# Kernel optimization log

Measured on AMD Instinct MI355X. Metric: run time of the kernel, lower is better.

## Reference

```python
import jax, jax.numpy as jnp
import numpy as np

EPS = 1e-8

def unit_projection(x):
    # project each embedding vector so its Fourier coefficients have unit magnitude
    f = jnp.fft.fft(x, axis=-1)
    f = f / jnp.maximum(jnp.abs(f), EPS)
    return jnp.real(jnp.fft.ifft(f, axis=-1))

def bind(a, b):
    return jnp.fft.irfft(jnp.fft.rfft(a, axis=-1) * jnp.fft.rfft(b, axis=-1), n=a.shape[-1], axis=-1)

def unbind(s, k):
    # k is unit-magnitude in Fourier domain, so its inverse is its conjugate
    return jnp.fft.irfft(jnp.fft.rfft(s, axis=-1) * jnp.conj(jnp.fft.rfft(k, axis=-1)), n=s.shape[-1], axis=-1)

def layer_norm(x, g, b):
    mu = jnp.mean(x, axis=-1, keepdims=True)
    var = jnp.var(x, axis=-1, keepdims=True)
    return (x - mu) * jax.lax.rsqrt(var + 1e-5) * g + b

def setup_inputs():
    key = jax.random.key(0)
    ks = jax.random.split(key, 12)
    B, S, D = 4, 2048, 1024
    sc = 1.0 / np.sqrt(D)
    inp = {
        'x': jax.random.normal(ks[0], (B, S, D), jnp.float32),
        'Wq': jax.random.normal(ks[1], (D, D), jnp.float32) * sc,
        'bq': jnp.zeros((D,), jnp.float32),
        'Wk': jax.random.normal(ks[2], (D, D), jnp.float32) * sc,
        'bk': jnp.zeros((D,), jnp.float32),
        'Wv': jax.random.normal(ks[3], (D, D), jnp.float32) * sc,
        'bv': jnp.zeros((D,), jnp.float32),
        'ln1_g': jnp.ones((D,), jnp.float32), 'ln1_b': jnp.zeros((D,), jnp.float32),
        'ln2_g': jnp.ones((D,), jnp.float32), 'ln2_b': jnp.zeros((D,), jnp.float32),
        'W1': jax.random.normal(ks[4], (D, 4 * D), jnp.float32) * sc,
        'b1': jnp.zeros((4 * D,), jnp.float32),
        'W2': jax.random.normal(ks[5], (4 * D, D), jnp.float32) * (1.0 / np.sqrt(4 * D)),
        'b2': jnp.zeros((D,), jnp.float32),
    }
    return inp

def reference(x, Wq, bq, Wk, bk, Wv, bv, ln1_g, ln1_b, ln2_g, ln2_b, W1, b1, W2, b2):
    h = layer_norm(x, ln1_g, ln1_b)
    q = unit_projection(h @ Wq + bq)
    k = unit_projection(h @ Wk + bk)
    v = unit_projection(h @ Wv + bv)
    s = jnp.cumsum(bind(k, v), axis=1)  # causal prefix-sum over sequence
    mixed = unbind(s, q)
    x = x + mixed  # dropout=0.0
    h2 = layer_norm(x, ln2_g, ln2_b)
    mlp = jax.nn.gelu(h2 @ W1 + b1, approximate=False) @ W2 + b2
    return x + mlp
```

## Files before the change

kernel.cpp:

```cpp
#include <hip/hip_runtime.h>
#include <cstdint>
#include <cstddef>

#define DD 1024
#define SSEQ 2048
#define NB 4
#define MROWS 8192
#define FBINS 513
#define FPAD 520
#define WFP 1152
#define NQKV 3456
#define NHID 4096
#define NCHUNK 64
#define SCHUNK 32

typedef _Float16 f16_t;
typedef _Float16 f16x8 __attribute__((ext_vector_type(8)));
typedef float f32x4 __attribute__((ext_vector_type(4)));

__device__ __forceinline__ float2 cmul(float2 a, float2 b) {
  return make_float2(a.x * b.x - a.y * b.y, a.x * b.y + a.y * b.x);
}

__device__ __forceinline__ void async_cp16(const void* g, void* l) {
  __builtin_amdgcn_global_load_lds(
      (const __attribute__((address_space(1))) void*)g,
      (__attribute__((address_space(3))) void*)l, 16, 0, 0);
}

__device__ __forceinline__ void fft1024(float2* bufA, float2* bufB,
                                        const float2* tw, int tid) {
  float2* s = bufA;
  float2* d = bufB;
  for (int m = 1; m < 1024; m <<= 1) {
#pragma unroll
    for (int r2 = 0; r2 < 2; ++r2) {
      int u = tid + r2 * 256;
      int k = u & (m - 1);
      int jm = u - k;
      float2 c0 = s[u];
      float2 c1 = s[u + 512];
      float2 wt = tw[jm];
      float2 su = make_float2(c0.x + c1.x, c0.y + c1.y);
      float2 df = make_float2(c0.x - c1.x, c0.y - c1.y);
      float2 pr = cmul(wt, df);
      d[2 * jm + k] = su;
      d[2 * jm + k + m] = pr;
    }
    __syncthreads();
    float2* tmp = s; s = d; d = tmp;
  }
}

__global__ __launch_bounds__(256) void wfft_k(
    const float* __restrict__ Wq, const float* __restrict__ Wk,
    const float* __restrict__ Wv, float* __restrict__ WfAll) {
  __shared__ float2 tw[512];
  __shared__ float2 bufA[1024];
  __shared__ float2 bufB[1024];
  const int tid = threadIdx.x;
  const int p = blockIdx.x >> 10, k = blockIdx.x & 1023;
  const float* W = (p == 0) ? Wq : ((p == 1) ? Wk : Wv);
  for (int t = tid; t < 512; t += 256) {
    float ang = -6.2831853071795864769f * (float)t * (1.0f / 1024.0f);
    tw[t] = make_float2(cosf(ang), sinf(ang));
  }
  const float* src = W + (size_t)k * DD;
  for (int t = tid; t < 1024; t += 256) bufA[t] = make_float2(src[t], 0.f);
  __syncthreads();
  fft1024(bufA, bufB, tw, tid);
  float* dst = WfAll + ((size_t)p * DD + k) * WFP;
  for (int t = tid; t <= 512; t += 256) {
    float2 f = bufA[t];
    dst[2 * t] = f.x;
    dst[2 * t + 1] = f.y;
  }
  for (int j = 1026 + tid; j < WFP; j += 256) dst[j] = 0.f;
}

__global__ __launch_bounds__(256) void bfft_k(
    const float* __restrict__ bq, const float* __restrict__ bk,
    const float* __restrict__ bv, float* __restrict__ biasC) {
  __shared__ float2 tw[512];
  __shared__ float2 bufA[1024];
  __shared__ float2 bufB[1024];
  const int tid = threadIdx.x;
  const int p = blockIdx.x;
  const float* bsrc = (p == 0) ? bq : ((p == 1) ? bk : bv);
  for (int t = tid; t < 512; t += 256) {
    float ang = -6.2831853071795864769f * (float)t * (1.0f / 1024.0f);
    tw[t] = make_float2(cosf(ang), sinf(ang));
  }
  for (int t = tid; t < 1024; t += 256) bufA[t] = make_float2(bsrc[t], 0.f);
  __syncthreads();
  fft1024(bufA, bufB, tw, tid);
  float* dst = biasC + (size_t)p * WFP;
  for (int t = tid; t <= 512; t += 256) {
    float2 f = bufA[t];
    dst[2 * t] = f.x;
    dst[2 * t + 1] = f.y;
  }
  for (int j = 1026 + tid; j < WFP; j += 256) dst[j] = 0.f;
}

__global__ __launch_bounds__(256) void transpose_cast_k(
    const float* __restrict__ W, f16_t* __restrict__ Wt, int K, int N) {
  __shared__ float tile[32][33];
  const int tx = threadIdx.x & 31, ty = threadIdx.x >> 5;
  const int n0 = blockIdx.x * 32, k0 = blockIdx.y * 32;
#pragma unroll
  for (int i = 0; i < 32; i += 8)
    tile[ty + i][tx] = W[(size_t)(k0 + ty + i) * N + n0 + tx];
  __syncthreads();
#pragma unroll
  for (int i = 0; i < 32; i += 8)
    Wt[(size_t)(n0 + ty + i) * K + k0 + tx] = (f16_t)tile[tx][ty + i];
}

__global__ __launch_bounds__(256) void transpose_cast2_k(
    const float* __restrict__ W, f16_t* __restrict__ WtH,
    f16_t* __restrict__ WtL, int K, int N) {
  __shared__ float tile[32][33];
  const int tx = threadIdx.x & 31, ty = threadIdx.x >> 5;
  const int n0 = blockIdx.x * 32, k0 = blockIdx.y * 32;
#pragma unroll
  for (int i = 0; i < 32; i += 8)
    tile[ty + i][tx] = W[(size_t)(k0 + ty + i) * N + n0 + tx];
  __syncthreads();
#pragma unroll
  for (int i = 0; i < 32; i += 8) {
    float val = tile[tx][ty + i];
    f16_t hi = (f16_t)val;
    f16_t lo = (f16_t)(val - (float)hi);
    size_t idx = (size_t)(n0 + ty + i) * K + k0 + tx;
    WtH[idx] = hi;
    WtL[idx] = lo;
  }
}

__global__ __launch_bounds__(256) void ln_cast2_k(
    const float* __restrict__ x, const float* __restrict__ g,
    const float* __restrict__ b, f16_t* __restrict__ hH,
    f16_t* __restrict__ hL) {
  const int row = blockIdx.x, tid = threadIdx.x;
  __shared__ float red[8];
  const float* xr = x + (size_t)row * DD;
  float v[4], ls = 0.f, lq = 0.f;
#pragma unroll
  for (int i = 0; i < 4; ++i) {
    v[i] = xr[i * 256 + tid];
    ls += v[i];
    lq += v[i] * v[i];
  }
#pragma unroll
  for (int o = 32; o > 0; o >>= 1) {
    ls += __shfl_down(ls, o);
    lq += __shfl_down(lq, o);
  }
  const int lane = tid & 63, w = tid >> 6;
  if (lane == 0) { red[w] = ls; red[w + 4] = lq; }
  __syncthreads();
  const float S = red[0] + red[1] + red[2] + red[3];
  const float Q = red[4] + red[5] + red[6] + red[7];
  const float mean = S * (1.f / 1024.f);
  const float var = Q * (1.f / 1024.f) - mean * mean;
  const float rs = rsqrtf(var + 1e-5f);
#pragma unroll
  for (int i = 0; i < 4; ++i) {
    int n = i * 256 + tid;
    float val = (v[i] - mean) * rs * g[n] + b[n];
    f16_t hi = (f16_t)val;
    hH[(size_t)row * DD + n] = hi;
    hL[(size_t)row * DD + n] = (f16_t)(val - (float)hi);
  }
}

__global__ __launch_bounds__(256, 2) void gemm_qkv_k(
    const f16_t* __restrict__ Ahi, const f16_t* __restrict__ Alo,
    const f16_t* __restrict__ Bhi, const float* __restrict__ bias,
    float* __restrict__ outF) {
  __shared__ alignas(16) f16_t AsH[128 * 64];
  __shared__ alignas(16) f16_t AsL[128 * 64];
  __shared__ alignas(16) f16_t BsH[128 * 64];
  const int tid = threadIdx.x;
  const int lane = tid & 63;
  const int w = tid >> 6;
  const int wm = w >> 1, wn = w & 1;

  const int lin = blockIdx.x;
  const int s = (lin & 7) * 216 + (lin >> 3);
  const int g = s / 108;
  const int r = s % 108;
  const int n = r >> 2;
  const int m0 = g * 4 + (r & 3);
  const int bn = n * 128;
  const int bm = m0 * 128;
  const bool qmode = (n < 9);

  f32x4 acc[4][4];
#pragma unroll
  for (int i = 0; i < 4; ++i)
#pragma unroll
    for (int j = 0; j < 4; ++j) acc[i][j] = (f32x4){0.f, 0.f, 0.f, 0.f};

  const int srow = lane >> 3;
  const int slot = lane & 7;

  for (int kt = 0; kt < 1024; kt += 64) {
#pragma unroll
    for (int i = 0; i < 4; ++i) {
      const int rb = (i * 4 + w) * 8;
      const int row = rb + srow;
      const int gg = (slot - (row & 7)) & 7;
      size_t ga = (size_t)(bm + row) * 1024 + kt + gg * 8;
      size_t gb = (size_t)(bn + row) * 1024 + kt + gg * 8;
      async_cp16(Ahi + ga, &AsH[rb * 64]);
      if (qmode) async_cp16(Alo + ga, &AsL[rb * 64]);
      async_cp16(Bhi + gb, &BsH[rb * 64]);
    }
    __syncthreads();
#pragma unroll
    for (int ks = 0; ks < 2; ++ks) {
      const int cgbase = ks * 4 + (lane >> 4);
      f16x8 ah[4], bh[4];
#pragma unroll
      for (int mt = 0; mt < 4; ++mt) {
        int m = wm * 64 + mt * 16 + (lane & 15);
        int sl = (cgbase + (m & 7)) & 7;
        ah[mt] = *(const f16x8*)(&AsH[m * 64 + sl * 8]);
      }
#pragma unroll
      for (int nt = 0; nt < 4; ++nt) {
        int nn = wn * 64 + nt * 16 + (lane & 15);
        int sl = (cgbase + (nn & 7)) & 7;
        bh[nt] = *(const f16x8*)(&BsH[nn * 64 + sl * 8]);
      }
#pragma unroll
      for (int mt = 0; mt < 4; ++mt)
#pragma unroll
        for (int nt = 0; nt < 4; ++nt)
          acc[mt][nt] = __builtin_amdgcn_mfma_f32_16x16x32_f16(
              ah[mt], bh[nt], acc[mt][nt], 0, 0, 0);
      if (qmode) {
        f16x8 al[4];
#pragma unroll
        for (int mt = 0; mt < 4; ++mt) {
          int m = wm * 64 + mt * 16 + (lane & 15);
          int sl = (cgbase + (m & 7)) & 7;
          al[mt] = *(const f16x8*)(&AsL[m * 64 + sl * 8]);
        }
#pragma unroll
        for (int mt = 0; mt < 4; ++mt)
#pragma unroll
          for (int nt = 0; nt < 4; ++nt)
            acc[mt][nt] = __builtin_amdgcn_mfma_f32_16x16x32_f16(
                al[mt], bh[nt], acc[mt][nt], 0, 0, 0);
      }
    }
    __syncthreads();
  }

  const int q = lane >> 4;
  const int cn = lane & 15;
#pragma unroll
  for (int mt = 0; mt < 4; ++mt) {
#pragma unroll
    for (int nt = 0; nt < 4; ++nt) {
      const int gcol = bn + wn * 64 + nt * 16 + cn;
      const float bv = bias[gcol];
      const int grow0 = bm + wm * 64 + mt * 16 + q * 4;
#pragma unroll
      for (int i = 0; i < 4; ++i) {
        size_t idx = (size_t)(grow0 + i) * NQKV + gcol;
        outF[idx] = acc[mt][nt][i] + bv;
      }
    }
  }
}

template <int EPI>
__global__ __launch_bounds__(256, 2) void gemm_bt_k(
    const f16_t* __restrict__ A, const f16_t* __restrict__ Bt,
    const float* __restrict__ bias, const float* __restrict__ resid,
    float* __restrict__ outF, f16_t* __restrict__ outH, int M, int N, int K) {
  __shared__ alignas(16) f16_t As[128 * 64];
  __shared__ alignas(16) f16_t Bs[128 * 64];
  const int tid = threadIdx.x;
  const int lane = tid & 63;
  const int w = tid >> 6;
  const int wm = w >> 1, wn = w & 1;
  int bm, bn;
  if (EPI == 2) {
    const int ntn = N >> 7;
    const int per = ((N >> 7) * (M >> 7)) >> 3;
    const int s = ((int)blockIdx.x & 7) * per + ((int)blockIdx.x >> 3);
    const int half = ntn * 2;
    const int g = s / half;
    const int r = s % half;
    bn = (r >> 1) * 128;
    bm = (g * 2 + (r & 1)) * 128;
  } else {
    bm = blockIdx.y * 128;
    bn = blockIdx.x * 128;
  }

  f32x4 acc[4][4];
#pragma unroll
  for (int i = 0; i < 4; ++i)
#pragma unroll
    for (int j = 0; j < 4; ++j) acc[i][j] = (f32x4){0.f, 0.f, 0.f, 0.f};

  const int srow = lane >> 3;
  const int slot = lane & 7;

  for (int kt = 0; kt < K; kt += 64) {
#pragma unroll
    for (int i = 0; i < 4; ++i) {
      const int rb = (i * 4 + w) * 8;
      const int row = rb + srow;
      const int gg = (slot - (row & 7)) & 7;
      const f16_t* ga = A + (size_t)(bm + row) * K + kt + gg * 8;
      const f16_t* gb = Bt + (size_t)(bn + row) * K + kt + gg * 8;
      async_cp16(ga, &As[rb * 64]);
      async_cp16(gb, &Bs[rb * 64]);
    }
    __syncthreads();
#pragma unroll
    for (int ks = 0; ks < 2; ++ks) {
      const int cgbase = ks * 4 + (lane >> 4);
      f16x8 af[4], bfv[4];
#pragma unroll
      for (int mt = 0; mt < 4; ++mt) {
        int m = wm * 64 + mt * 16 + (lane & 15);
        int sl = (cgbase + (m & 7)) & 7;
        af[mt] = *(const f16x8*)(&As[m * 64 + sl * 8]);
      }
#pragma unroll
      for (int nt = 0; nt < 4; ++nt) {
        int nn = wn * 64 + nt * 16 + (lane & 15);
        int sl = (cgbase + (nn & 7)) & 7;
        bfv[nt] = *(const f16x8*)(&Bs[nn * 64 + sl * 8]);
      }
#pragma unroll
      for (int mt = 0; mt < 4; ++mt)
#pragma unroll
        for (int nt = 0; nt < 4; ++nt)
          acc[mt][nt] = __builtin_amdgcn_mfma_f32_16x16x32_f16(
              af[mt], bfv[nt], acc[mt][nt], 0, 0, 0);
    }
    __syncthreads();
  }

  const int q = lane >> 4;
  const int cn = lane & 15;
#pragma unroll
  for (int mt = 0; mt < 4; ++mt) {
#pragma unroll
    for (int nt = 0; nt < 4; ++nt) {
      const int gcol = bn + wn * 64 + nt * 16 + cn;
      const float bv = bias[gcol];
      const int grow0 = bm + wm * 64 + mt * 16 + q * 4;
#pragma unroll
      for (int i = 0; i < 4; ++i) {
        float val = acc[mt][nt][i] + bv;
        size_t idx = (size_t)(grow0 + i) * N + gcol;
        if (EPI == 1) {
          float ge = 0.5f * val * (1.0f + erff(val * 0.70710678118654752f));
          outH[idx] = (f16_t)ge;
        } else {
          outF[idx] = val + resid[idx];
        }
      }
    }
  }
}

__device__ __forceinline__ float2 unitc(float2 a) {
  float inv = 1.0f / fmaxf(sqrtf(a.x * a.x + a.y * a.y), 1e-8f);
  return make_float2(a.x * inv, a.y * inv);
}
__device__ __forceinline__ float2 bind_bin(const float2* r, int f) {
  float2 kn = unitc(r[576 + f]);
  float2 vn = unitc(r[1152 + f]);
  return cmul(kn, vn);
}

__global__ __launch_bounds__(256) void scan_pass1_k(
    const float* __restrict__ qkvF, float2* __restrict__ T) {
  const int b = blockIdx.x >> 6, sc = blockIdx.x & 63;
  const int s0 = sc * SCHUNK;
  const float2* base = (const float2*)(qkvF + ((size_t)(b * SSEQ + s0)) * NQKV);
  for (int f = threadIdx.x; f < FBINS; f += 256) {
    float2 acc = make_float2(0.f, 0.f);
    const float2* r = base;
    for (int i = 0; i < SCHUNK; ++i) {
      float2 pv = bind_bin(r, f);
      acc.x += pv.x; acc.y += pv.y;
      r += NQKV / 2;
    }
    T[((size_t)b * NCHUNK + sc) * FBINS + f] = acc;
  }
}

__global__ void scan_pass2_k(float2* __restrict__ T) {
  const int idx = blockIdx.x * 256 + threadIdx.x;
  if (idx >= NB * FBINS) return;
  const int b = idx / FBINS, f = idx % FBINS;
  float2 acc = make_float2(0.f, 0.f);
  for (int sc = 0; sc < NCHUNK; ++sc) {
    size_t a = ((size_t)b * NCHUNK + sc) * FBINS + f;
    float2 v = T[a];
    T[a] = acc;
    acc.x += v.x; acc.y += v.y;
  }
}

__global__ __launch_bounds__(256) void scan_pass3_k(
    const float* __restrict__ qkvF, const float2* __restrict__ T,
    float2* __restrict__ Scum) {
  const int b = blockIdx.x >> 6, sc = blockIdx.x & 63;
  const int s0 = sc * SCHUNK;
  const float2* base = (const float2*)(qkvF + ((size_t)(b * SSEQ + s0)) * NQKV);
  for (int f = threadIdx.x; f < FBINS; f += 256) {
    float2 acc = T[((size_t)b * NCHUNK + sc) * FBINS + f];
    const float2* r = base;
    size_t orow = ((size_t)(b * SSEQ + s0)) * FPAD + f;
    for (int i = 0; i < SCHUNK; ++i) {
      float2 pv = bind_bin(r, f);
      acc.x += pv.x; acc.y += pv.y;
      Scum[orow] = acc;
      r += NQKV / 2;
      orow += FPAD;
    }
  }
}

__global__ __launch_bounds__(256) void unbind_ln2_k(
    const float2* __restrict__ Scum, const float* __restrict__ qkvF,
    const float* __restrict__ x, float* __restrict__ x2out,
    f16_t* __restrict__ h2, const float* __restrict__ g2,
    const float* __restrict__ b2) {
  __shared__ float2 tw[512];
  __shared__ float2 bufA[1024];
  __shared__ float2 bufB[1024];
  __shared__ float red[8];
  const int tid = threadIdx.x;
  const int row = blockIdx.x;

  for (int t = tid; t < 512; t += 256) {
    float ang = 6.2831853071795864769f * (float)t * (1.0f / 1024.0f);
    tw[t] = make_float2(cosf(ang), sinf(ang));
  }
  const float2* qrow = (const float2*)(qkvF + (size_t)row * NQKV);
  for (int t = tid; t <= 512; t += 256) {
    float2 sc = Scum[(size_t)row * FPAD + t];
    float2 fq = unitc(qrow[t]);
    float2 Mv = make_float2(sc.x * fq.x + sc.y * fq.y, sc.y * fq.x - sc.x * fq.y);
    bufA[t] = Mv;
    if (t >= 1 && t < 512) bufA[1024 - t] = make_float2(Mv.x, -Mv.y);
  }
  __syncthreads();
  fft1024(bufA, bufB, tw, tid);

  const float* xr = x + (size_t)row * DD;
  float v[4], ls = 0.f, lq = 0.f;
#pragma unroll
  for (int i = 0; i < 4; ++i) {
    int n = i * 256 + tid;
    float val = xr[n] + bufA[n].x * (1.0f / 1024.0f);
    x2out[(size_t)row * DD + n] = val;
    v[i] = val;
    ls += val;
    lq += val * val;
  }
#pragma unroll
  for (int o = 32; o > 0; o >>= 1) {
    ls += __shfl_down(ls, o);
    lq += __shfl_down(lq, o);
  }
  const int lane = tid & 63, w = tid >> 6;
  if (lane == 0) { red[w] = ls; red[w + 4] = lq; }
  __syncthreads();
  const float S = red[0] + red[1] + red[2] + red[3];
  const float Q = red[4] + red[5] + red[6] + red[7];
  const float mean = S * (1.f / 1024.f);
  const float var = Q * (1.f / 1024.f) - mean * mean;
  const float rs = rsqrtf(var + 1e-5f);
  f16_t* hr = h2 + (size_t)row * DD;
#pragma unroll
  for (int i = 0; i < 4; ++i) {
    int n = i * 256 + tid;
    hr[n] = (f16_t)((v[i] - mean) * rs * g2[n] + b2[n]);
  }
}

extern "C" void kernel_launch(void* const* d_in, const int* in_sizes, int n_in,
                              void* d_out, int out_size, void* d_ws,
                              size_t ws_size, hipStream_t stream) {
  const float* x     = (const float*)d_in[0];
  const float* Wq    = (const float*)d_in[1];
  const float* bq    = (const float*)d_in[2];
  const float* Wk    = (const float*)d_in[3];
  const float* bk    = (const float*)d_in[4];
  const float* Wv    = (const float*)d_in[5];
  const float* bv    = (const float*)d_in[6];
  const float* ln1_g = (const float*)d_in[7];
  const float* ln1_b = (const float*)d_in[8];
  const float* ln2_g = (const float*)d_in[9];
  const float* ln2_b = (const float*)d_in[10];
  const float* W1    = (const float*)d_in[11];
  const float* b1    = (const float*)d_in[12];
  const float* W2    = (const float*)d_in[13];
  const float* b2    = (const float*)d_in[14];
  float* out = (float*)d_out;

  char* p = (char*)d_ws;
  auto take = [&](size_t bytes) {
    char* r = p;
    p += (bytes + 255) & ~(size_t)255;
    return r;
  };
  f16_t* BtH   = (f16_t*)take((size_t)NQKV * DD * sizeof(f16_t));
  f16_t* BtL   = (f16_t*)take((size_t)NQKV * DD * sizeof(f16_t));
  f16_t* W1T   = (f16_t*)take((size_t)NHID * DD * sizeof(f16_t));
  f16_t* W2T   = (f16_t*)take((size_t)DD * NHID * sizeof(f16_t));
  float* biasC = (float*)take((size_t)NQKV * sizeof(float));
  f16_t* hbuf  = (f16_t*)take((size_t)MROWS * DD * sizeof(f16_t));
  char*  big   = take((size_t)MROWS * NQKV * sizeof(float));
  float2* Scum = (float2*)take((size_t)MROWS * FPAD * sizeof(float2));
  float* x2    = (float*)take((size_t)MROWS * DD * sizeof(float));
  float2* Tch  = (float2*)take((size_t)NB * NCHUNK * FBINS * sizeof(float2));
  float* WfAll   = (float*)big;
  float* qkv_f   = (float*)big;
  f16_t* mlp1    = (f16_t*)big;
  f16_t* hlo     = (f16_t*)x2;

  wfft_k<<<3 * DD, 256, 0, stream>>>(Wq, Wk, Wv, WfAll);
  for (int pp = 0; pp < 3; ++pp)
    transpose_cast2_k<<<dim3(WFP / 32, DD / 32), 256, 0, stream>>>(
        WfAll + (size_t)pp * DD * WFP,
        BtH + (size_t)pp * WFP * DD,
        BtL + (size_t)pp * WFP * DD, DD, WFP);
  bfft_k<<<3, 256, 0, stream>>>(bq, bk, bv, biasC);
  transpose_cast_k<<<dim3(128, 32), 256, 0, stream>>>(W1, W1T, DD, NHID);
  transpose_cast_k<<<dim3(32, 128), 256, 0, stream>>>(W2, W2T, NHID, DD);

  ln_cast2_k<<<MROWS, 256, 0, stream>>>(x, ln1_g, ln1_b, hbuf, hlo);

  gemm_qkv_k<<<(NQKV / 128) * (MROWS / 128), 256, 0, stream>>>(
      hbuf, hlo, BtH, biasC, qkv_f);

  scan_pass1_k<<<NB * NCHUNK, 256, 0, stream>>>(qkv_f, Tch);
  scan_pass2_k<<<(NB * FBINS + 255) / 256, 256, 0, stream>>>(Tch);
  scan_pass3_k<<<NB * NCHUNK, 256, 0, stream>>>(qkv_f, Tch, Scum);

  unbind_ln2_k<<<MROWS, 256, 0, stream>>>(Scum, qkv_f, x, x2, hbuf, ln2_g, ln2_b);

  gemm_bt_k<1><<<dim3(NHID / 128, MROWS / 128), 256, 0, stream>>>(
      hbuf, W1T, b1, nullptr, nullptr, mlp1, MROWS, NHID, DD);

  gemm_bt_k<2><<<(DD / 128) * (MROWS / 128), 256, 0, stream>>>(
      mlp1, W2T, b2, x2, out, nullptr, MROWS, DD, NHID);
}
```

Baseline: 570.3 us.

## Use half-length complex FFT for real inverse, fast GELU, split scan blocks

Three separate changes. The inverse real FFT in unbind_ln2 is now a 512-point complex FFT over packed even/odd outputs plus a twiddle pre-step, where it used to be a full 1024-point complex FFT over a Hermitian-extended buffer. This halves the LDS butterfly stages' work, and the x/gamma/beta loads and h2 stores become float2/f16x2 vectors. The GELU epilogue replaces erff with the Abramowitz-Stegun polynomial using rcp and exp2 intrinsics, which is an approximation with error near 1e-7. The scan passes split the frequency bins across two blocks, doubling the grid to 512 blocks so more of the GPU is occupied.

```diff
diff --git a/kernel.cpp b/kernel.cpp
--- a/kernel.cpp
+++ b/kernel.cpp
@@ -16,6 +16,7 @@
 
 typedef _Float16 f16_t;
 typedef _Float16 f16x8 __attribute__((ext_vector_type(8)));
+typedef _Float16 f16x2 __attribute__((ext_vector_type(2)));
 typedef float f32x4 __attribute__((ext_vector_type(4)));
 
 __device__ __forceinline__ float2 cmul(float2 a, float2 b) {
@@ -26,6 +27,20 @@
   __builtin_amdgcn_global_load_lds(
       (const __attribute__((address_space(1))) void*)g,
       (__attribute__((address_space(3))) void*)l, 16, 0, 0);
+}
+
+__device__ __forceinline__ float fast_gelu(float val) {
+  float av = __builtin_fabsf(val);
+  float z = av * 0.70710678118654752f;
+  float t = __builtin_amdgcn_rcpf(__builtin_fmaf(0.3275911f, z, 1.0f));
+  float poly = t * __builtin_fmaf(t,
+      __builtin_fmaf(t, __builtin_fmaf(t,
+          __builtin_fmaf(t, 1.061405429f, -1.453152027f),
+          1.421413741f), -0.284496736f), 0.254829592f);
+  float e = __builtin_amdgcn_exp2f(z * z * -1.4426950408889634f);
+  float w = poly * e;
+  float r = fmaxf(val, 0.0f);
+  return __builtin_fmaf(-0.5f * av, w, r);
 }
 
 __device__ __forceinline__ void fft1024(float2* bufA, float2* bufB,
@@ -50,6 +65,28 @@
     __syncthreads();
     float2* tmp = s; s = d; d = tmp;
   }
+}
+
+__device__ __forceinline__ float2* fft512(float2* bufA, float2* bufB,
+                                          const float2* tw, int tid) {
+  float2* s = bufA;
+  float2* d = bufB;
+  for (int m = 1; m < 512; m <<= 1) {
+    int u = tid;
+    int k = u & (m - 1);
+    int jm = u - k;
+    float2 c0 = s[u];
+    float2 c1 = s[u + 256];
+    float2 wt = tw[jm];
+    float2 su = make_float2(c0.x + c1.x, c0.y + c1.y);
+    float2 df = make_float2(c0.x - c1.x, c0.y - c1.y);
+    float2 pr = cmul(wt, df);
+    d[2 * jm + k] = su;
+    d[2 * jm + k + m] = pr;
+    __syncthreads();
+    float2* tmp = s; s = d; d = tmp;
+  }
+  return s;
 }
 
 __global__ __launch_bounds__(256) void wfft_k(
@@ -365,8 +402,7 @@
         float val = acc[mt][nt][i] + bv;
         size_t idx = (size_t)(grow0 + i) * N + gcol;
         if (EPI == 1) {
-          float ge = 0.5f * val * (1.0f + erff(val * 0.70710678118654752f));
-          outH[idx] = (f16_t)ge;
+          outH[idx] = (f16_t)fast_gelu(val);
         } else {
           outF[idx] = val + resid[idx];
         }
@@ -387,10 +423,13 @@
 
 __global__ __launch_bounds__(256) void scan_pass1_k(
     const float* __restrict__ qkvF, float2* __restrict__ T) {
-  const int b = blockIdx.x >> 6, sc = blockIdx.x & 63;
+  const int bid = blockIdx.x;
+  const int sc = bid & 63;
+  const int fh = (bid >> 6) & 1;
+  const int b = bid >> 7;
   const int s0 = sc * SCHUNK;
   const float2* base = (const float2*)(qkvF + ((size_t)(b * SSEQ + s0)) * NQKV);
-  for (int f = threadIdx.x; f < FBINS; f += 256) {
+  for (int f = fh * 256 + threadIdx.x; f < FBINS; f += 512) {
     float2 acc = make_float2(0.f, 0.f);
     const float2* r = base;
     for (int i = 0; i < SCHUNK; ++i) {
@@ -418,10 +457,13 @@
 __global__ __launch_bounds__(256) void scan_pass3_k(
     const float* __restrict__ qkvF, const float2* __restrict__ T,
     float2* __restrict__ Scum) {
-  const int b = blockIdx.x >> 6, sc = blockIdx.x & 63;
+  const int bid = blockIdx.x;
+  const int sc = bid & 63;
+  const int fh = (bid >> 6) & 1;
+  const int b = bid >> 7;
   const int s0 = sc * SCHUNK;
   const float2* base = (const float2*)(qkvF + ((size_t)(b * SSEQ + s0)) * NQKV);
-  for (int f = threadIdx.x; f < FBINS; f += 256) {
+  for (int f = fh * 256 + threadIdx.x; f < FBINS; f += 512) {
     float2 acc = T[((size_t)b * NCHUNK + sc) * FBINS + f];
     const float2* r = base;
     size_t orow = ((size_t)(b * SSEQ + s0)) * FPAD + f;
@@ -440,38 +482,54 @@
     const float* __restrict__ x, float* __restrict__ x2out,
     f16_t* __restrict__ h2, const float* __restrict__ g2,
     const float* __restrict__ b2) {
-  __shared__ float2 tw[512];
-  __shared__ float2 bufA[1024];
-  __shared__ float2 bufB[1024];
+  __shared__ float2 tw[256];
+  __shared__ float2 Marr[513];
+  __shared__ float2 bufA[512];
+  __shared__ float2 bufB[512];
   __shared__ float red[8];
   const int tid = threadIdx.x;
   const int row = blockIdx.x;
 
-  for (int t = tid; t < 512; t += 256) {
-    float ang = 6.2831853071795864769f * (float)t * (1.0f / 1024.0f);
-    tw[t] = make_float2(cosf(ang), sinf(ang));
+  {
+    float ang = 6.2831853071795864769f * (float)tid * (1.0f / 512.0f);
+    tw[tid] = make_float2(cosf(ang), sinf(ang));
   }
   const float2* qrow = (const float2*)(qkvF + (size_t)row * NQKV);
   for (int t = tid; t <= 512; t += 256) {
     float2 sc = Scum[(size_t)row * FPAD + t];
     float2 fq = unitc(qrow[t]);
-    float2 Mv = make_float2(sc.x * fq.x + sc.y * fq.y, sc.y * fq.x - sc.x * fq.y);
-    bufA[t] = Mv;
-    if (t >= 1 && t < 512) bufA[1024 - t] = make_float2(Mv.x, -Mv.y);
-  }
-  __syncthreads();
-  fft1024(bufA, bufB, tw, tid);
+    Marr[t] = make_float2(sc.x * fq.x + sc.y * fq.y, sc.y * fq.x - sc.x * fq.y);
+  }
+  __syncthreads();
+#pragma unroll
+  for (int rr = 0; rr < 2; ++rr) {
+    int t = tid + rr * 256;
+    float2 a = Marr[t];
+    float2 b = Marr[512 - t];
+    float2 E = make_float2(0.5f * (a.x + b.x), 0.5f * (a.y - b.y));
+    float2 Dd = make_float2(0.5f * (a.x - b.x), 0.5f * (a.y + b.y));
+    float ang = 6.2831853071795864769f * (float)t * (1.0f / 1024.0f);
+    float cw = cosf(ang), sw = sinf(ang);
+    float2 O = make_float2(cw * Dd.x - sw * Dd.y, cw * Dd.y + sw * Dd.x);
+    bufA[t] = make_float2(E.x - O.y, E.y + O.x);
+  }
+  __syncthreads();
+  float2* res = fft512(bufA, bufB, tw, tid);
 
   const float* xr = x + (size_t)row * DD;
-  float v[4], ls = 0.f, lq = 0.f;
-#pragma unroll
-  for (int i = 0; i < 4; ++i) {
-    int n = i * 256 + tid;
-    float val = xr[n] + bufA[n].x * (1.0f / 1024.0f);
-    x2out[(size_t)row * DD + n] = val;
-    v[i] = val;
-    ls += val;
-    lq += val * val;
+  float v[2][2];
+  float ls = 0.f, lq = 0.f;
+#pragma unroll
+  for (int rr = 0; rr < 2; ++rr) {
+    int n = tid + rr * 256;
+    float2 z = res[n];
+    float2 xv = *(const float2*)(xr + 2 * n);
+    float v0 = xv.x + z.x * (1.0f / 512.0f);
+    float v1 = xv.y + z.y * (1.0f / 512.0f);
+    *(float2*)(x2out + (size_t)row * DD + 2 * n) = make_float2(v0, v1);
+    v[rr][0] = v0; v[rr][1] = v1;
+    ls += v0 + v1;
+    lq += v0 * v0 + v1 * v1;
   }
 #pragma unroll
   for (int o = 32; o > 0; o >>= 1) {
@@ -488,9 +546,14 @@
   const float rs = rsqrtf(var + 1e-5f);
   f16_t* hr = h2 + (size_t)row * DD;
 #pragma unroll
-  for (int i = 0; i < 4; ++i) {
-    int n = i * 256 + tid;
-    hr[n] = (f16_t)((v[i] - mean) * rs * g2[n] + b2[n]);
+  for (int rr = 0; rr < 2; ++rr) {
+    int n = tid + rr * 256;
+    float2 gv = *(const float2*)(g2 + 2 * n);
+    float2 bv = *(const float2*)(b2 + 2 * n);
+    f16x2 hp;
+    hp[0] = (f16_t)((v[rr][0] - mean) * rs * gv.x + bv.x);
+    hp[1] = (f16_t)((v[rr][1] - mean) * rs * gv.y + bv.y);
+    *(f16x2*)(hr + 2 * n) = hp;
   }
 }
 
@@ -550,9 +613,9 @@
   gemm_qkv_k<<<(NQKV / 128) * (MROWS / 128), 256, 0, stream>>>(
       hbuf, hlo, BtH, biasC, qkv_f);
 
-  scan_pass1_k<<<NB * NCHUNK, 256, 0, stream>>>(qkv_f, Tch);
+  scan_pass1_k<<<NB * NCHUNK * 2, 256, 0, stream>>>(qkv_f, Tch);
   scan_pass2_k<<<(NB * FBINS + 255) / 256, 256, 0, stream>>>(Tch);
-  scan_pass3_k<<<NB * NCHUNK, 256, 0, stream>>>(qkv_f, Tch, Scum);
+  scan_pass3_k<<<NB * NCHUNK * 2, 256, 0, stream>>>(qkv_f, Tch, Scum);
 
   unbind_ln2_k<<<MROWS, 256, 0, stream>>>(Scum, qkv_f, x, x2, hbuf, ln2_g, ln2_b);
 
```

Result: faster. 534.3 us (-6.3%).
